# Kernel tuning notes

Measured on AMD Instinct MI355X. Metric: run time of the kernel, lower is better.

## Reference

```python
import jax, jax.numpy as jnp
import numpy as np

EPS = 1e-6  # torch.nn.PairwiseDistance default eps, added to the difference vector


def setup_inputs() -> dict:
    key = jax.random.key(0)
    k1, k2, k3 = jax.random.split(key, 3)
    B, L1, L2, D = 4, 4096, 4096, 3
    contour1 = jax.random.normal(k1, (B, L1, D), dtype=jnp.float32)
    contour2 = jax.random.normal(k2, (B, L2, D), dtype=jnp.float32)
    resolution = jax.random.uniform(k3, (1,), dtype=jnp.float32)
    return {"contour1": contour1, "contour2": contour2, "resolution": resolution}


def reference(contour1, contour2, resolution):
    # torch PairwiseDistance(2): dist = ||x1 - x2 + eps||_2 with x1 from contour1,
    # x2 from contour2. Expand ||c1 - c2 + eps||^2 =
    #   ||c1||^2 + ||c2||^2 - 2 c1.c2 + 2*eps*(sum(c1) - sum(c2)) + D*eps^2
    # to avoid materializing the [B, L2, L1, D] repeated tensors.
    D = contour1.shape[-1]
    s1 = jnp.sum(contour1 * contour1, axis=-1)          # [B, L1]
    s2 = jnp.sum(contour2 * contour2, axis=-1)          # [B, L2]
    sum1 = jnp.sum(contour1, axis=-1)                   # [B, L1]
    sum2 = jnp.sum(contour2, axis=-1)                   # [B, L2]
    cross = jnp.einsum('bmd,bld->bml', contour2, contour1)  # [B, L2, L1]
    dist2 = (s2[:, :, None] + s1[:, None, :] - 2.0 * cross
             + 2.0 * EPS * (sum1[:, None, :] - sum2[:, :, None])
             + D * EPS * EPS)
    dist = jnp.sqrt(jnp.maximum(dist2, 0.0))            # [B, L2, L1]
    min_dist = jnp.min(dist, axis=2)                    # [B, L2]
    return jnp.mean(min_dist * resolution, axis=1)      # [B]
```

## Files before the change

kernel.cpp:

```cpp
#include <hip/hip_runtime.h>
#include <math.h>

#define EPS 1e-6f
#define FLT_BIG 3.402823466e+38f

constexpr int BLK = 256;
constexpr int MPT = 4;
constexpr int NCHUNK = 32;
constexpr int MAXCL = 256;
constexpr int RBLK = 1024;

__global__ void __launch_bounds__(BLK)
k_min(const float* __restrict__ c1, const float* __restrict__ c2,
      float* __restrict__ part, int L1, int L2, int CL) {
    __shared__ float4 tile[MAXCL];

    const int b = blockIdx.z;
    const int chunk = blockIdx.y;
    const int l0 = chunk * CL;
    const int nl = min(CL, L1 - l0);

    const float* src = c1 + ((size_t)b * L1 + l0) * 3;
    for (int i = threadIdx.x; i < nl; i += BLK) {
        float x = src[3 * i], y = src[3 * i + 1], z = src[3 * i + 2];
        tile[i] = make_float4(fmaf(x, x, fmaf(y, y, z * z)),
                              -2.0f * x, -2.0f * y, -2.0f * z);
    }
    __syncthreads();

    const int mbase = blockIdx.x * (BLK * MPT) + threadIdx.x;

    float q0[MPT], q1[MPT], q2[MPT], mn[MPT];
    #pragma unroll
    for (int j = 0; j < MPT; ++j) {
        const int m = mbase + j * BLK;
        if (m < L2) {
            const float* q = c2 + ((size_t)b * L2 + m) * 3;
            q0[j] = q[0] - EPS; q1[j] = q[1] - EPS; q2[j] = q[2] - EPS;
        } else {
            q0[j] = q1[j] = q2[j] = 0.0f;
        }
        mn[j] = FLT_BIG;
    }

    int l = 0;
    #pragma unroll 2
    for (; l + 2 <= nl; l += 2) {
        float4 pa = tile[l], pb = tile[l + 1];
        #pragma unroll
        for (int j = 0; j < MPT; ++j) {
            float ta = fmaf(pa.w, q2[j], fmaf(pa.z, q1[j], fmaf(pa.y, q0[j], pa.x)));
            float tb = fmaf(pb.w, q2[j], fmaf(pb.z, q1[j], fmaf(pb.y, q0[j], pb.x)));
            mn[j] = fminf(mn[j], fminf(ta, tb));
        }
    }
    for (; l < nl; ++l) {
        float4 p = tile[l];
        #pragma unroll
        for (int j = 0; j < MPT; ++j) {
            float t = fmaf(p.w, q2[j], fmaf(p.z, q1[j], fmaf(p.y, q0[j], p.x)));
            mn[j] = fminf(mn[j], t);
        }
    }

    float* dst = part + ((size_t)b * NCHUNK + chunk) * L2;
    #pragma unroll
    for (int j = 0; j < MPT; ++j) {
        const int m = mbase + j * BLK;
        if (m < L2) {
            const float qq = fmaf(q0[j], q0[j], fmaf(q1[j], q1[j], q2[j] * q2[j]));
            dst[m] = mn[j] + qq;
        }
    }
}

__global__ void __launch_bounds__(RBLK)
k_reduce(const float* __restrict__ part, const float* __restrict__ res,
         float* __restrict__ out, int L2) {
    const int b = blockIdx.x;

    float sum = 0.0f;
    for (int m = threadIdx.x; m < L2; m += RBLK) {
        float v = FLT_BIG;
        #pragma unroll
        for (int c = 0; c < NCHUNK; ++c)
            v = fminf(v, part[((size_t)b * NCHUNK + c) * L2 + m]);
        sum += sqrtf(fmaxf(v, 0.0f));
    }

    #pragma unroll
    for (int s = 32; s > 0; s >>= 1)
        sum += __shfl_down(sum, s, 64);

    __shared__ float wred[RBLK / 64];
    const int wid = threadIdx.x >> 6;
    const int lane = threadIdx.x & 63;
    if (lane == 0) wred[wid] = sum;
    __syncthreads();

    if (threadIdx.x == 0) {
        float tot = 0.0f;
        #pragma unroll
        for (int w = 0; w < RBLK / 64; ++w) tot += wred[w];
        out[b] = tot * res[0] / (float)L2;
    }
}

extern "C" void kernel_launch(void* const* d_in, const int* in_sizes, int n_in,
                              void* d_out, int out_size, void* d_ws, size_t ws_size,
                              hipStream_t stream) {
    const float* c1  = (const float*)d_in[0];
    const float* c2  = (const float*)d_in[1];
    const float* res = (const float*)d_in[2];
    float* out = (float*)d_out;

    const int B = out_size;
    const int D = 3;
    const int L1 = in_sizes[0] / (B * D);
    const int L2 = in_sizes[1] / (B * D);

    float* part = (float*)d_ws;

    const int CL = (L1 + NCHUNK - 1) / NCHUNK;
    dim3 g1((L2 + BLK * MPT - 1) / (BLK * MPT), NCHUNK, B);
    k_min<<<g1, BLK, 0, stream>>>(c1, c2, part, L1, L2, CL);

    k_reduce<<<B, RBLK, 0, stream>>>(part, res, out, L2);
}
```

Baseline: 21.43 us.

## Fuse min and reduction kernels using last-block atomic counters

Merges the chunked min kernel and the separate reduce kernel into one launch. Each block bumps an atomic counter after writing its partial minima, and the last block per m-range finishes the cross-chunk min, sqrt and block sum. A second counter lets the last of those blocks combine the per-range sums into the output. This removes a kernel launch and the serial single-block-per-batch reduction, at the cost of a memset, threadfences and atomics. NMB is hardcoded to 4, so the code assumes L2 fits in 4*BLK*MPT.

```diff
diff --git a/kernel.cpp b/kernel.cpp
--- a/kernel.cpp
+++ b/kernel.cpp
@@ -7,28 +7,33 @@
 constexpr int BLK = 256;
 constexpr int MPT = 4;
 constexpr int NCHUNK = 32;
+constexpr int NMB = 4;
 constexpr int MAXCL = 256;
-constexpr int RBLK = 1024;
 
 __global__ void __launch_bounds__(BLK)
-k_min(const float* __restrict__ c1, const float* __restrict__ c2,
-      float* __restrict__ part, int L1, int L2, int CL) {
+k_all(const float* __restrict__ c1, const float* __restrict__ c2,
+      const float* __restrict__ res, float* __restrict__ part,
+      float* __restrict__ psum, int* __restrict__ cntA, int* __restrict__ cntB,
+      float* __restrict__ out, int L1, int L2, int CL) {
     __shared__ float4 tile[MAXCL];
+    __shared__ float red[BLK];
+    __shared__ int flag;
 
-    const int b = blockIdx.z;
-    const int chunk = blockIdx.y;
+    const int mb = blockIdx.x, chunk = blockIdx.y, b = blockIdx.z;
+    const int tid = threadIdx.x;
+
     const int l0 = chunk * CL;
     const int nl = min(CL, L1 - l0);
 
     const float* src = c1 + ((size_t)b * L1 + l0) * 3;
-    for (int i = threadIdx.x; i < nl; i += BLK) {
+    for (int i = tid; i < nl; i += BLK) {
         float x = src[3 * i], y = src[3 * i + 1], z = src[3 * i + 2];
         tile[i] = make_float4(fmaf(x, x, fmaf(y, y, z * z)),
                               -2.0f * x, -2.0f * y, -2.0f * z);
     }
     __syncthreads();
 
-    const int mbase = blockIdx.x * (BLK * MPT) + threadIdx.x;
+    const int mbase = mb * (BLK * MPT) + tid;
 
     float q0[MPT], q1[MPT], q2[MPT], mn[MPT];
     #pragma unroll
@@ -57,10 +62,8 @@
     for (; l < nl; ++l) {
         float4 p = tile[l];
         #pragma unroll
-        for (int j = 0; j < MPT; ++j) {
-            float t = fmaf(p.w, q2[j], fmaf(p.z, q1[j], fmaf(p.y, q0[j], p.x)));
-            mn[j] = fminf(mn[j], t);
-        }
+        for (int j = 0; j < MPT; ++j)
+            mn[j] = fminf(mn[j], fmaf(p.w, q2[j], fmaf(p.z, q1[j], fmaf(p.y, q0[j], p.x))));
     }
 
     float* dst = part + ((size_t)b * NCHUNK + chunk) * L2;
@@ -72,37 +75,43 @@
             dst[m] = mn[j] + qq;
         }
     }
-}
 
-__global__ void __launch_bounds__(RBLK)
-k_reduce(const float* __restrict__ part, const float* __restrict__ res,
-         float* __restrict__ out, int L2) {
-    const int b = blockIdx.x;
+    __threadfence();
+    if (tid == 0) flag = atomicAdd(&cntA[b * NMB + mb], 1);
+    __syncthreads();
+    if (flag != NCHUNK - 2) return;
+    __threadfence();
 
     float sum = 0.0f;
-    for (int m = threadIdx.x; m < L2; m += RBLK) {
-        float v = FLT_BIG;
-        #pragma unroll
-        for (int c = 0; c < NCHUNK; ++c)
-            v = fminf(v, part[((size_t)b * NCHUNK + c) * L2 + m]);
-        sum += sqrtf(fmaxf(v, 0.0f));
+    #pragma unroll
+    for (int j = 0; j < MPT; ++j) {
+        const int m = mbase + j * BLK;
+        if (m < L2) {
+            float v = FLT_BIG;
+            #pragma unroll 8
+            for (int c = 0; c < NCHUNK; ++c)
+                v = fminf(v, part[((size_t)b * NCHUNK + c) * L2 + m]);
+            sum += sqrtf(fmaxf(v, 0.0f));
+        }
+    }
+    red[tid] = sum;
+    __syncthreads();
+    for (int s = BLK / 2; s > 0; s >>= 1) {
+        if (tid < s) red[tid] += red[tid + s];
+        __syncthreads();
     }
 
-    #pragma unroll
-    for (int s = 32; s > 0; s >>= 1)
-        sum += __shfl_down(sum, s, 64);
-
-    __shared__ float wred[RBLK / 64];
-    const int wid = threadIdx.x >> 6;
-    const int lane = threadIdx.x & 63;
-    if (lane == 0) wred[wid] = sum;
-    __syncthreads();
-
-    if (threadIdx.x == 0) {
-        float tot = 0.0f;
-        #pragma unroll
-        for (int w = 0; w < RBLK / 64; ++w) tot += wred[w];
-        out[b] = tot * res[0] / (float)L2;
+    if (tid == 0) {
+        psum[b * NMB + mb] = red[0];
+        __threadfence();
+        int old = atomicAdd(&cntB[b], 1);
+        if (old == NMB - 2) {
+            __threadfence();
+            float s = 0.0f;
+            #pragma unroll
+            for (int k = 0; k < NMB; ++k) s += psum[b * NMB + k];
+            out[b] = s * res[0] / (float)L2;
+        }
     }
 }
 
@@ -120,10 +129,14 @@
     const int L2 = in_sizes[1] / (B * D);
 
     float* part = (float*)d_ws;
+    float* psum = part + (size_t)B * NCHUNK * L2;
+    int*   cntA = (int*)(psum + B * NMB);
+    int*   cntB = cntA + B * NMB;
+
+    hipMemsetAsync(cntA, 0xFF, (size_t)(B * NMB + B) * sizeof(int), stream);
 
     const int CL = (L1 + NCHUNK - 1) / NCHUNK;
-    dim3 g1((L2 + BLK * MPT - 1) / (BLK * MPT), NCHUNK, B);
-    k_min<<<g1, BLK, 0, stream>>>(c1, c2, part, L1, L2, CL);
-
-    k_reduce<<<B, RBLK, 0, stream>>>(part, res, out, L2);
+    dim3 grid(NMB, NCHUNK, B);
+    k_all<<<grid, BLK, 0, stream>>>(c1, c2, res, part, psum, cntA, cntB,
+                                    out, L1, L2, CL);
 }
```

Result: slower. 74.36 us (+247.1%).

## Widen final reduction across blocks with atomics and specialize min kernel to fixed chunks

Applied to the files above, without the earlier changes.

Replaces the 4-block final reduction with a grid of 256-thread blocks. Each block does the chunk-min, sqrt and a block sum for its points, then adds the result into the output with atomicAdd; the output is zeroed by the first min-kernel block. The min kernel now uses 8 query points per thread, a fixed 128-point chunk and no bounds checks, which halves the number of blocks and raises per-thread reuse of each shared tile. This assumes L1 equals NCHUNK*128 and that L2 is a multiple of the tile sizes, and it makes the float summation order nondeterministic.

```diff
diff --git a/kernel.cpp b/kernel.cpp
--- a/kernel.cpp
+++ b/kernel.cpp
@@ -5,47 +5,42 @@
 #define FLT_BIG 3.402823466e+38f
 
 constexpr int BLK = 256;
-constexpr int MPT = 4;
+constexpr int MPT = 8;
 constexpr int NCHUNK = 32;
-constexpr int MAXCL = 256;
-constexpr int RBLK = 1024;
+constexpr int NMB = 2;
+constexpr int CLK = 128;
 
 __global__ void __launch_bounds__(BLK)
 k_min(const float* __restrict__ c1, const float* __restrict__ c2,
-      float* __restrict__ part, int L1, int L2, int CL) {
-    __shared__ float4 tile[MAXCL];
+      float* __restrict__ part, float* __restrict__ out, int L1, int L2) {
+    __shared__ float4 tile[CLK];
 
-    const int b = blockIdx.z;
-    const int chunk = blockIdx.y;
-    const int l0 = chunk * CL;
-    const int nl = min(CL, L1 - l0);
+    const int mb = blockIdx.x, chunk = blockIdx.y, b = blockIdx.z;
+    const int tid = threadIdx.x;
 
+    if (mb == 0 && chunk == 0 && tid == 0) out[b] = 0.0f;
+
+    const int l0 = chunk * CLK;
     const float* src = c1 + ((size_t)b * L1 + l0) * 3;
-    for (int i = threadIdx.x; i < nl; i += BLK) {
-        float x = src[3 * i], y = src[3 * i + 1], z = src[3 * i + 2];
-        tile[i] = make_float4(fmaf(x, x, fmaf(y, y, z * z)),
-                              -2.0f * x, -2.0f * y, -2.0f * z);
+    if (tid < CLK) {
+        float x = src[3 * tid], y = src[3 * tid + 1], z = src[3 * tid + 2];
+        tile[tid] = make_float4(fmaf(x, x, fmaf(y, y, z * z)),
+                                -2.0f * x, -2.0f * y, -2.0f * z);
     }
     __syncthreads();
 
-    const int mbase = blockIdx.x * (BLK * MPT) + threadIdx.x;
+    const int mbase = mb * (BLK * MPT) + tid;
 
     float q0[MPT], q1[MPT], q2[MPT], mn[MPT];
     #pragma unroll
     for (int j = 0; j < MPT; ++j) {
-        const int m = mbase + j * BLK;
-        if (m < L2) {
-            const float* q = c2 + ((size_t)b * L2 + m) * 3;
-            q0[j] = q[0] - EPS; q1[j] = q[1] - EPS; q2[j] = q[2] - EPS;
-        } else {
-            q0[j] = q1[j] = q2[j] = 0.0f;
-        }
+        const float* q = c2 + ((size_t)b * L2 + mbase + j * BLK) * 3;
+        q0[j] = q[0] - EPS; q1[j] = q[1] - EPS; q2[j] = q[2] - EPS;
         mn[j] = FLT_BIG;
     }
 
-    int l = 0;
     #pragma unroll 2
-    for (; l + 2 <= nl; l += 2) {
+    for (int l = 0; l < CLK; l += 2) {
         float4 pa = tile[l], pb = tile[l + 1];
         #pragma unroll
         for (int j = 0; j < MPT; ++j) {
@@ -54,55 +49,41 @@
             mn[j] = fminf(mn[j], fminf(ta, tb));
         }
     }
-    for (; l < nl; ++l) {
-        float4 p = tile[l];
-        #pragma unroll
-        for (int j = 0; j < MPT; ++j) {
-            float t = fmaf(p.w, q2[j], fmaf(p.z, q1[j], fmaf(p.y, q0[j], p.x)));
-            mn[j] = fminf(mn[j], t);
-        }
-    }
 
     float* dst = part + ((size_t)b * NCHUNK + chunk) * L2;
     #pragma unroll
     for (int j = 0; j < MPT; ++j) {
-        const int m = mbase + j * BLK;
-        if (m < L2) {
-            const float qq = fmaf(q0[j], q0[j], fmaf(q1[j], q1[j], q2[j] * q2[j]));
-            dst[m] = mn[j] + qq;
-        }
+        const float qq = fmaf(q0[j], q0[j], fmaf(q1[j], q1[j], q2[j] * q2[j]));
+        dst[mbase + j * BLK] = mn[j] + qq;
     }
 }
 
-__global__ void __launch_bounds__(RBLK)
-k_reduce(const float* __restrict__ part, const float* __restrict__ res,
-         float* __restrict__ out, int L2) {
-    const int b = blockIdx.x;
+__global__ void __launch_bounds__(BLK)
+k_tail(const float* __restrict__ part, const float* __restrict__ res,
+       float* __restrict__ out, int L2) {
+    const int b = blockIdx.y;
+    const int m = blockIdx.x * BLK + threadIdx.x;
 
-    float sum = 0.0f;
-    for (int m = threadIdx.x; m < L2; m += RBLK) {
-        float v = FLT_BIG;
-        #pragma unroll
-        for (int c = 0; c < NCHUNK; ++c)
-            v = fminf(v, part[((size_t)b * NCHUNK + c) * L2 + m]);
-        sum += sqrtf(fmaxf(v, 0.0f));
-    }
+    float v = FLT_BIG;
+    #pragma unroll 8
+    for (int c = 0; c < NCHUNK; ++c)
+        v = fminf(v, part[((size_t)b * NCHUNK + c) * L2 + m]);
+    float sum = sqrtf(fmaxf(v, 0.0f));
 
     #pragma unroll
     for (int s = 32; s > 0; s >>= 1)
         sum += __shfl_down(sum, s, 64);
 
-    __shared__ float wred[RBLK / 64];
+    __shared__ float wred[BLK / 64];
     const int wid = threadIdx.x >> 6;
-    const int lane = threadIdx.x & 63;
-    if (lane == 0) wred[wid] = sum;
+    if ((threadIdx.x & 63) == 0) wred[wid] = sum;
     __syncthreads();
 
     if (threadIdx.x == 0) {
         float tot = 0.0f;
         #pragma unroll
-        for (int w = 0; w < RBLK / 64; ++w) tot += wred[w];
-        out[b] = tot * res[0] / (float)L2;
+        for (int w = 0; w < BLK / 64; ++w) tot += wred[w];
+        atomicAdd(&out[b], tot * res[0] / (float)L2);
     }
 }
 
@@ -121,9 +102,9 @@
 
     float* part = (float*)d_ws;
 
-    const int CL = (L1 + NCHUNK - 1) / NCHUNK;
-    dim3 g1((L2 + BLK * MPT - 1) / (BLK * MPT), NCHUNK, B);
-    k_min<<<g1, BLK, 0, stream>>>(c1, c2, part, L1, L2, CL);
+    dim3 g1(NMB, NCHUNK, B);
+    k_min<<<g1, BLK, 0, stream>>>(c1, c2, part, out, L1, L2);
 
-    k_reduce<<<B, RBLK, 0, stream>>>(part, res, out, L2);
+    dim3 g2(L2 / BLK, B);
+    k_tail<<<g2, BLK, 0, stream>>>(part, res, out, L2);
 }
```

New measurement: 19.30 us. 9.9% less time.
